# Kernel tuning notes

Hardware: AMD Instinct MI355X
Metric: run time of the kernel (lower is better)

Reference implementation:

```python
import jax, jax.numpy as jnp
import numpy as np

N_NODES = 20000
N_EDGES = 640000
IN_DIM = 128
HEADS = 4
C1 = 64      # hidden_dim1
C2 = 128     # hidden_dim2 (gat2, 1 head)
GRU = 128
PW = 15      # pred_window


def gat_layer(x, src, dst, W, a_src, a_dst, bias):
    # PyG GATConv (eval mode, self-loops already appended): linear -> per-edge
    # LeakyReLU(0.2) attention -> segment softmax over dst -> scatter-sum.
    n = x.shape[0]
    heads, ch = a_src.shape
    xl = (x @ W).reshape(n, heads, ch)                      # [N,H,C]
    al = jnp.sum(xl * a_src, axis=-1)                       # [N,H]
    ar = jnp.sum(xl * a_dst, axis=-1)                       # [N,H]
    e = jax.nn.leaky_relu(al[src] + ar[dst], 0.2)           # [E,H]
    m = jax.ops.segment_max(e, dst, num_segments=n)
    ee = jnp.exp(e - m[dst])
    s = jax.ops.segment_sum(ee, dst, num_segments=n)
    alpha = ee / s[dst]                                     # [E,H]
    msg = xl[src] * alpha[:, :, None]                       # [E,H,C]
    out = jax.ops.segment_sum(msg, dst, num_segments=n)
    return out.reshape(n, heads * ch) + bias


def gru_cell(x, h, W_ih, W_hh, b_ih, b_hh):
    gi = x @ W_ih.T + b_ih
    gh = h @ W_hh.T + b_hh
    ir, iz, ih = jnp.split(gi, 3, axis=1)
    hr, hz, hn = jnp.split(gh, 3, axis=1)
    r = jax.nn.sigmoid(ir + hr)
    z = jax.nn.sigmoid(iz + hz)
    n = jnp.tanh(ih + r * hn)
    return (1.0 - z) * n + z * h


def setup_inputs() -> dict:
    key = jax.random.key(0)
    ks = jax.random.split(key, 24)
    f = jnp.float32
    sc = 0.05
    inp = {
        'dynamic': jax.random.normal(ks[0], (N_NODES, IN_DIM), dtype=f),
        'edge_index': jax.random.randint(ks[1], (2, N_EDGES), 0, N_NODES, dtype=jnp.int32),
        'cI': jax.random.uniform(ks[2], (N_NODES,), dtype=f),
        'cR': jax.random.uniform(ks[3], (N_NODES,), dtype=f),
        'Npop': jnp.ones((N_NODES, 1), dtype=f) * 1e6,
        'I': jax.random.uniform(ks[4], (N_NODES,), dtype=f) * 100.0,
        'R': jax.random.uniform(ks[5], (N_NODES,), dtype=f) * 100.0,
        'dI': jax.random.normal(ks[6], (N_NODES,), dtype=f),
        'dR': jax.random.normal(ks[7], (N_NODES,), dtype=f),
        # gat1
        'W1': jax.random.normal(ks[8], (IN_DIM, HEADS * C1), dtype=f) * sc,
        'a_src1': jax.random.normal(ks[9], (HEADS, C1), dtype=f) * sc,
        'a_dst1': jax.random.normal(ks[10], (HEADS, C1), dtype=f) * sc,
        'b1': jnp.zeros((HEADS * C1,), dtype=f),
        # gat2 (1 head)
        'W2': jax.random.normal(ks[11], (HEADS * C1, C2), dtype=f) * sc,
        'a_src2': jax.random.normal(ks[12], (1, C2), dtype=f) * sc,
        'a_dst2': jax.random.normal(ks[13], (1, C2), dtype=f) * sc,
        'b2': jnp.zeros((C2,), dtype=f),
        # GRUCell
        'W_ih': jax.random.normal(ks[14], (3 * GRU, C2), dtype=f) * sc,
        'W_hh': jax.random.normal(ks[15], (3 * GRU, GRU), dtype=f) * sc,
        'b_ih': jnp.zeros((3 * GRU,), dtype=f),
        'b_hh': jnp.zeros((3 * GRU,), dtype=f),
        # output heads
        'W_I': jax.random.normal(ks[16], (PW, GRU + 2), dtype=f) * sc,
        'b_I': jnp.zeros((PW,), dtype=f),
        'W_R': jax.random.normal(ks[17], (PW, GRU + 2), dtype=f) * sc,
        'b_R': jnp.zeros((PW,), dtype=f),
        'W_sir': jax.random.normal(ks[18], (2, GRU + 2), dtype=f) * sc,
        'b_sir': jnp.zeros((2,), dtype=f),
    }
    return inp


def reference(dynamic, edge_index, cI, cR, Npop, I, R, dI, dR,
              W1, a_src1, a_dst1, b1, W2, a_src2, a_dst2, b2,
              W_ih, W_hh, b_ih, b_hh, W_I, b_I, W_R, b_R, W_sir, b_sir):
    n = dynamic.shape[0]
    loops = jnp.arange(n, dtype=edge_index.dtype)
    src = jnp.concatenate([edge_index[0], loops])   # PyG add_self_loops=True
    dst = jnp.concatenate([edge_index[1], loops])

    x = jax.nn.elu(gat_layer(dynamic, src, dst, W1, a_src1, a_dst1, b1))
    x = jax.nn.elu(gat_layer(x, src, dst, W2, a_src2, a_dst2, b2))

    h = gru_cell(x, jnp.zeros((n, GRU), dtype=x.dtype), W_ih, W_hh, b_ih, b_hh)
    hc = jnp.concatenate([h, cI[:, None], cR[:, None]], axis=1)
    pred_I = hc @ W_I.T + b_I
    pred_R = hc @ W_R.T + b_R
    pred_res = hc @ W_sir.T + b_sir
    alpha = jax.nn.sigmoid(pred_res[:, 0])
    beta = jax.nn.sigmoid(pred_res[:, 1])

    Nv = Npop[:, 0]
    S = Nv - I - R
    phy_I, phy_R = [], []
    for _ in range(PW):
        dI_val = alpha * I * (S / Nv) - beta * I
        dR_val = beta * I
        phy_I.append(dI_val)
        phy_R.append(dR_val)
        I = I + jax.lax.stop_gradient(dI_val)
        R = R + jax.lax.stop_gradient(dR_val)
    phy_I = jnp.stack(phy_I, axis=1)
    phy_R = jnp.stack(phy_R, axis=1)
    return pred_I, pred_R, phy_I, phy_R, h
```

## Files before the change

kernel.cpp:

```cpp
#include <hip/hip_runtime.h>

#define NN 20000
#define NE 640000
#define NET (NE + NN)
#define NB 128
#define RR 157
#define NSL 256
#define ESL4 625

typedef __attribute__((ext_vector_type(8))) short bf16x8;
typedef __attribute__((ext_vector_type(4))) float f32x4;
typedef __attribute__((ext_vector_type(2))) float f32x2;

__device__ inline ushort f2bf_rne(float x) {
    unsigned u = __float_as_uint(x);
    return (ushort)((u + 0x7FFFu + ((u >> 16) & 1u)) >> 16);
}
__device__ inline float bf2f(ushort u) {
    return __uint_as_float(((unsigned)u) << 16);
}
__device__ inline void split2(float x, ushort& hi, ushort& lo) {
    unsigned u = __float_as_uint(x);
    unsigned r = (u + 0x7FFFu + ((u >> 16) & 1u)) & 0xFFFF0000u;
    hi = (ushort)(r >> 16);
    lo = f2bf_rne(x - __uint_as_float(r));
}
__device__ inline float rlane(float x, int k) {
    return __int_as_float(__builtin_amdgcn_readlane(__float_as_int(x), k));
}


__global__ void csrA_kernel(const int* __restrict__ ei, int* __restrict__ cnt,
                            const float* __restrict__ W1, const float* __restrict__ as1,
                            const float* __restrict__ ad1, float* __restrict__ w1f,
                            const float* __restrict__ W2, const float* __restrict__ as2,
                            const float* __restrict__ ad2, float* __restrict__ w2f,
                            const float* __restrict__ W_ih,
                            const float* __restrict__ W_I, const float* __restrict__ b_I,
                            const float* __restrict__ W_R, const float* __restrict__ b_R,
                            const float* __restrict__ W_sir, const float* __restrict__ b_sir,
                            ushort* __restrict__ w1fh, ushort* __restrict__ w1fl,
                            ushort* __restrict__ w2fh, ushort* __restrict__ w2fl,
                            ushort* __restrict__ w3fh, ushort* __restrict__ w3fl,
                            ushort* __restrict__ wtfh, ushort* __restrict__ wtfl,
                            float* __restrict__ wc, float* __restrict__ wb) {
    int b = blockIdx.x, t = threadIdx.x;
    if (b < NSL) {
        __shared__ int h[NB];
        if (t < NB) h[t] = 0;
        __syncthreads();
        const int4* d4 = (const int4*)(ei + NE);
        for (int i = t; i < ESL4; i += 256) {
            int4 d = d4[b * ESL4 + i];
            atomicAdd(&h[(unsigned)d.x / RR], 1);
            atomicAdd(&h[(unsigned)d.y / RR], 1);
            atomicAdd(&h[(unsigned)d.z / RR], 1);
            atomicAdd(&h[(unsigned)d.w / RR], 1);
        }
        __syncthreads();
        if (t < NB) cnt[t * NSL + b] = h[t];
    } else if (b == NSL) {
        if (t < 128) {
            int k = t;
#pragma unroll
            for (int hh = 0; hh < 4; hh++) {
                float s1 = 0.f, s2 = 0.f;
                for (int c = 0; c < 64; c++) {
                    float w = W1[k * 256 + hh * 64 + c];
                    s1 += w * as1[hh * 64 + c];
                    s2 += w * ad1[hh * 64 + c];
                }
                w1f[k * 8 + hh] = s1;
                w1f[k * 8 + 4 + hh] = s2;
            }
        }
    } else if (b == NSL + 1) {
        int k = t;
        float s1 = 0.f, s2 = 0.f;
        for (int c = 0; c < 128; c++) {
            float w = W2[k * 128 + c];
            s1 += w * as2[c];
            s2 += w * ad2[c];
        }
        w2f[k * 2] = s1;
        w2f[k * 2 + 1] = s2;
    } else if (b == NSL + 2) {
        if (t < 32) {
            int p = t;
            const float* Wr = (p < 15) ? W_I + p * 130
                            : (p < 30) ? W_R + (p - 15) * 130
                                       : W_sir + (p - 30) * 130;
            wc[p * 2] = Wr[128];
            wc[p * 2 + 1] = Wr[129];
            wb[p] = (p < 15) ? b_I[p] : (p < 30) ? b_R[p - 15] : b_sir[p - 30];
        }
    } else {
        int pb = b - (NSL + 3);
        if (pb < 16) {
            int base = pb * 2048;
#pragma unroll
            for (int q = 0; q < 8; q++) {
                int i = base + t + q * 256;
                int j = i & 7, ln = (i >> 3) & 63, rem = i >> 9;
                int k32 = rem & 3, n16 = rem >> 2;
                int k = k32 * 32 + ((ln >> 4) << 3) + j;
                int n = n16 * 16 + (ln & 15);
                ushort h, l; split2(W1[k * 256 + n], h, l);
                w1fh[i] = h; w1fl[i] = l;
            }
        } else if (pb < 32) {
            int base = (pb - 16) * 2048;
#pragma unroll
            for (int q = 0; q < 8; q++) {
                int i = base + t + q * 256;
                int j = i & 7, ln = (i >> 3) & 63, rem = i >> 9;
                int k32 = rem & 7, n16 = rem >> 3;
                int k = k32 * 32 + ((ln >> 4) << 3) + j;
                int n = n16 * 16 + (ln & 15);
                ushort h, l; split2(W2[k * 128 + n], h, l);
                w2fh[i] = h; w2fl[i] = l;
            }
        } else if (pb < 56) {
            int base = (pb - 32) * 2048;
#pragma unroll
            for (int q = 0; q < 8; q++) {
                int i = base + t + q * 256;
                int j = i & 7, ln = (i >> 3) & 63, rem = i >> 9;
                int k32 = rem & 3, n16 = rem >> 2;
                int k = k32 * 32 + ((ln >> 4) << 3) + j;
                int n = n16 * 16 + (ln & 15);
                ushort h, l; split2(W_ih[n * 128 + k], h, l);
                w3fh[i] = h; w3fl[i] = l;
            }
        } else {
            int base = (pb - 56) * 2048;
#pragma unroll
            for (int q = 0; q < 8; q++) {
                int i = base + t + q * 256;
                int j = i & 7, ln = (i >> 3) & 63, rem = i >> 9;
                int k32 = rem & 3, n16 = rem >> 2;
                int k = k32 * 32 + ((ln >> 4) << 3) + j;
                int n = n16 * 16 + (ln & 15);
                const float* Wr = (n < 15) ? W_I + n * 130
                                : (n < 30) ? W_R + (n - 15) * 130
                                           : W_sir + (n - 30) * 130;
                ushort h, l; split2(Wr[k], h, l);
                wtfh[i] = h; wtfl[i] = l;
            }
        }
    }
}

__global__ void csrB_kernel(const int* __restrict__ cnt, int* __restrict__ sbase) {
    __shared__ int ws1[16], ws2[16];
    int t = threadIdx.x, wv = t >> 6, ln = t & 63;
    int base = t * 32;
    int loc[32];
    int run = 0;
#pragma unroll
    for (int q = 0; q < 32; q++) { loc[q] = run; run += cnt[base + q]; }
    int s = run;
#pragma unroll
    for (int o = 1; o < 64; o <<= 1) { int u = __shfl_up(s, o, 64); if (ln >= o) s += u; }
    if (ln == 63) ws1[wv] = s;
    __syncthreads();
    if (t < 16) {
        int sv = ws1[t];
#pragma unroll
        for (int o = 1; o < 16; o <<= 1) { int u = __shfl_up(sv, o, 16); if (t >= o) sv += u; }
        ws2[t] = sv;
    }
    __syncthreads();
    int excl = (wv ? ws2[wv - 1] : 0) + s - run;
#pragma unroll
    for (int q = 0; q < 32; q++) sbase[base + q] = excl + loc[q];
}

__global__ void csrC_kernel(const int* __restrict__ ei, const int* __restrict__ sbase,
                            int* __restrict__ ebuf, const float* __restrict__ X,
                            const float* __restrict__ wf, ushort* __restrict__ Xbf,
                            float* __restrict__ al, float* __restrict__ ar) {
    int b = blockIdx.x, t = threadIdx.x;
    if (b < NSL) {
        __shared__ int cur[NB];
        if (t < NB) cur[t] = sbase[t * NSL + b];
        __syncthreads();
        const int4* s4 = (const int4*)ei;
        const int4* d4 = (const int4*)(ei + NE);
        for (int i = t; i < ESL4; i += 256) {
            int4 sv = s4[b * ESL4 + i];
            int4 dv = d4[b * ESL4 + i];
            int p;
            p = atomicAdd(&cur[(unsigned)dv.x / RR], 1); ebuf[p] = sv.x | (dv.x << 15);
            p = atomicAdd(&cur[(unsigned)dv.y / RR], 1); ebuf[p] = sv.y | (dv.y << 15);
            p = atomicAdd(&cur[(unsigned)dv.z / RR], 1); ebuf[p] = sv.z | (dv.z << 15);
            p = atomicAdd(&cur[(unsigned)dv.w / RR], 1); ebuf[p] = sv.w | (dv.w << 15);
        }
    } else {
        __shared__ float ws[8][128];
        for (int i = t; i < 1024; i += 256) ws[i & 7][i >> 3] = wf[i];
        __syncthreads();
        int wv = t >> 6, ln = t & 63;
        int n = (b - NSL) * 4 + wv;
        float2 xv = *(const float2*)(X + (size_t)n * 128 + ln * 2);
        ushort2 ub;
        ub.x = f2bf_rne(xv.x);
        ub.y = f2bf_rne(xv.y);
        *(ushort2*)(Xbf + (size_t)n * 128 + ln * 2) = ub;
        float p[8];
#pragma unroll
        for (int o = 0; o < 8; o++) p[o] = xv.x * ws[o][ln * 2] + xv.y * ws[o][ln * 2 + 1];
#pragma unroll
        for (int off = 32; off > 0; off >>= 1)
#pragma unroll
            for (int o = 0; o < 8; o++) p[o] += __shfl_xor(p[o], off, 64);
        if (ln == 0) {
#pragma unroll
            for (int h = 0; h < 4; h++) {
                al[n * 4 + h] = p[h];
                ar[n * 4 + h] = p[4 + h];
            }
        }
    }
}

__global__ void csrD_kernel(const int* __restrict__ ebuf, const int* __restrict__ sbase,
                            int* __restrict__ offs, int* __restrict__ csr_src) {
    __shared__ int hist[RR], lcur[RR];
    int b = blockIdx.x, t = threadIdx.x;
    int lo = b * RR;
    int Ra = min(RR, NN - lo);
    int e0 = sbase[b * NSL];
    int e1 = (b < NB - 1) ? sbase[(b + 1) * NSL] : NE;
    int m = e1 - e0;
    for (int i = t; i < Ra; i += 256) hist[i] = 0;
    __syncthreads();
    for (int j = t; j < m; j += 256) atomicAdd(&hist[(ebuf[e0 + j] >> 15) - lo], 1);
    __syncthreads();
    if (t < 64) {
        int cbase = e0 + lo;
        int carry = 0;
#pragma unroll
        for (int c = 0; c < 3; c++) {
            int i = c * 64 + t;
            int v = (i < Ra) ? hist[i] + 1 : 0;
            int s = v;
#pragma unroll
            for (int o = 1; o < 64; o <<= 1) { int u = __shfl_up(s, o, 64); if (t >= o) s += u; }
            if (i < Ra) {
                int off = cbase + carry + s - v;
                offs[lo + i] = off;
                lcur[i] = off;
            }
            carry += __shfl(s, 63, 64);
        }
    }
    if (b == 0 && t == 255) offs[NN] = NET;
    __syncthreads();
    for (int i = t; i < Ra; i += 256) csr_src[lcur[i] + hist[i]] = lo + i;
    __syncthreads();
    for (int j = t; j < m; j += 256) {
        int p = ebuf[e0 + j];
        int pos = atomicAdd(&lcur[(p >> 15) - lo], 1);
        csr_src[pos] = p & 0x7FFF;
    }
}

template <int H, bool FUSE>
__launch_bounds__(256)
__global__ void gat_gather_w(const ushort* __restrict__ X, const float* __restrict__ al,
                             const float* __restrict__ ar, const int* __restrict__ offs,
                             const int* __restrict__ csr, const float* __restrict__ bias,
                             void* __restrict__ outp) {
    int t = threadIdx.x;
    int wv = t >> 6, ln = t & 63;
    int n = blockIdx.x * 4 + wv;
    int e0 = offs[n], e1 = offs[n + 1];

    float arv[H], srun[H];
    f32x2 acc2[H];
#pragma unroll
    for (int h = 0; h < H; h++) {
        arv[h] = ar[n * H + h];
        srun[h] = 0.f;
        acc2[h][0] = 0.f; acc2[h][1] = 0.f;
    }
    const ushort* Xc = X + ln * 2;

    for (int base = e0; base < e1; base += 64) {
        int cnt = e1 - base; if (cnt > 64) cnt = 64;
        bool vld = ln < cnt;
        int src = vld ? csr[base + ln] : 0;
        float wgt[H];
        {
            float av[H];
            if (H == 4) {
                float4 a4 = *(const float4*)(al + (size_t)src * 4);
                av[0] = a4.x; av[H > 1 ? 1 : 0] = a4.y;
                av[H > 2 ? 2 : 0] = a4.z; av[H > 3 ? 3 : 0] = a4.w;
            } else {
                av[0] = al[src];
            }
#pragma unroll
            for (int h = 0; h < H; h++) {
                float lg = av[h] + arv[h];
                lg = lg > 0.f ? lg : 0.2f * lg;
                wgt[h] = vld ? __expf(lg) : 0.f;
            }
        }
        float ls[H];
#pragma unroll
        for (int h = 0; h < H; h++) ls[h] = wgt[h];
#pragma unroll
        for (int off = 32; off > 0; off >>= 1)
#pragma unroll
            for (int h = 0; h < H; h++) ls[h] += __shfl_xor(ls[h], off, 64);
#pragma unroll
        for (int h = 0; h < H; h++) srun[h] += ls[h];

        int k = 0;
        for (; k + 16 <= cnt; k += 16) {
            int s[16];
            unsigned u[16];
#pragma unroll
            for (int q = 0; q < 16; q++) s[q] = __builtin_amdgcn_readlane(src, k + q);
#pragma unroll
            for (int q = 0; q < 16; q++) u[q] = *(const unsigned*)(Xc + (size_t)s[q] * 128);
#pragma unroll
            for (int q = 0; q < 16; q++) {
                f32x2 xv;
                xv[0] = __uint_as_float(u[q] << 16);
                xv[1] = __uint_as_float(u[q] & 0xffff0000u);
#pragma unroll
                for (int h = 0; h < H; h++) {
                    float w = rlane(wgt[h], k + q);
                    f32x2 ww; ww[0] = w; ww[1] = w;
                    acc2[h] = __builtin_elementwise_fma(ww, xv, acc2[h]);
                }
            }
        }
        for (; k + 8 <= cnt; k += 8) {
            int s[8];
            unsigned u[8];
#pragma unroll
            for (int q = 0; q < 8; q++) s[q] = __builtin_amdgcn_readlane(src, k + q);
#pragma unroll
            for (int q = 0; q < 8; q++) u[q] = *(const unsigned*)(Xc + (size_t)s[q] * 128);
#pragma unroll
            for (int q = 0; q < 8; q++) {
                f32x2 xv;
                xv[0] = __uint_as_float(u[q] << 16);
                xv[1] = __uint_as_float(u[q] & 0xffff0000u);
#pragma unroll
                for (int h = 0; h < H; h++) {
                    float w = rlane(wgt[h], k + q);
                    f32x2 ww; ww[0] = w; ww[1] = w;
                    acc2[h] = __builtin_elementwise_fma(ww, xv, acc2[h]);
                }
            }
        }
        for (; k < cnt; k++) {
            int s0 = __builtin_amdgcn_readlane(src, k);
            unsigned u0 = *(const unsigned*)(Xc + (size_t)s0 * 128);
            f32x2 xv;
            xv[0] = __uint_as_float(u0 << 16);
            xv[1] = __uint_as_float(u0 & 0xffff0000u);
#pragma unroll
            for (int h = 0; h < H; h++) {
                float w = rlane(wgt[h], k);
                f32x2 ww; ww[0] = w; ww[1] = w;
                acc2[h] = __builtin_elementwise_fma(ww, xv, acc2[h]);
            }
        }
    }
    if (FUSE) {
        ushort* out = (ushort*)outp;
        float inv = 1.f / srun[0];
        float v0 = acc2[0][0] * inv + bias[ln * 2];
        float v1 = acc2[0][1] * inv + bias[ln * 2 + 1];
        v0 = v0 > 0.f ? v0 : __expf(v0) - 1.f;
        v1 = v1 > 0.f ? v1 : __expf(v1) - 1.f;
        ushort2 o;
        o.x = f2bf_rne(v0);
        o.y = f2bf_rne(v1);
        *(ushort2*)(out + (size_t)n * 128 + ln * 2) = o;
    } else {
        ushort* out = (ushort*)outp;
#pragma unroll
        for (int h = 0; h < H; h++) {
            float inv = 1.f / srun[h];
            ushort2 o;
            o.x = f2bf_rne(acc2[h][0] * inv);
            o.y = f2bf_rne(acc2[h][1] * inv);
            *(ushort2*)(out + (size_t)n * (H * 128) + h * 128 + ln * 2) = o;
        }
    }
}

template <int ACT, bool OUTBF, int BN, bool ALAR>
__launch_bounds__(256)
__global__ void gemm_fr(const ushort* __restrict__ A, const ushort* __restrict__ Bfh,
                        const ushort* __restrict__ Bfl, const float* __restrict__ bias,
                        void* __restrict__ Cptr, int M, int K, int lda, int ldc,
                        int zA, int zB, int zC, const float* __restrict__ w2f,
                        float* __restrict__ al2, float* __restrict__ ar2) {
    constexpr int NF = BN / 32;
    __shared__ ushort Ah[128 * 64];
    __shared__ float s_w2f[ALAR ? 256 : 1][2];
    int tid = threadIdx.x;
    int z = blockIdx.z;
    int bm = blockIdx.x * 128;
    int ny = blockIdx.y * BN;
    int wid = tid >> 6, ln = tid & 63;
    int wm = wid >> 1, wn = wid & 1;
    int K32v = K >> 5;
    const bf16x8* BfhV = (const bf16x8*)Bfh;
    const bf16x8* BflV = (const bf16x8*)Bfl;
    f32x4 acc[4][NF];
#pragma unroll
    for (int a = 0; a < 4; a++)
#pragma unroll
        for (int b = 0; b < NF; b++)
#pragma unroll
            for (int j = 0; j < 4; j++) acc[a][b][j] = 0.f;
    float p0a[8], p1a[8];
    if (ALAR) {
#pragma unroll
        for (int i = 0; i < 8; i++) { p0a[i] = 0.f; p1a[i] = 0.f; }
        s_w2f[tid][0] = w2f[tid * 2];
        s_w2f[tid][1] = w2f[tid * 2 + 1];
        __syncthreads();
    }
    size_t abase = (size_t)z * zA;
    int bcb = z * zB + ny;
    int ct[NF];
#pragma unroll
    for (int nf = 0; nf < NF; nf++) ct[nf] = (bcb + wn * (BN / 2) + nf * 16) >> 4;

    for (int k0 = 0; k0 < K; k0 += 64) {
#pragma unroll
        for (int i = 0; i < 8; i++) {
            int idx = tid + i * 256;
            int r = idx >> 4, c4 = (idx & 15) * 4;
            int gr = bm + r;
            ushort4 v = make_ushort4(0, 0, 0, 0);
            if (gr < M) v = *(const ushort4*)(A + abase + (size_t)gr * lda + k0 + c4);
            int ab = (r * 128 + c4 * 2) ^ ((r & 7) << 4);
            *(ushort4*)((char*)Ah + ab) = v;
            if (ALAR) {
                int kk = k0 + c4;
                float x0 = bf2f(v.x), x1 = bf2f(v.y), x2 = bf2f(v.z), x3 = bf2f(v.w);
                p0a[i] = fmaf(x0, s_w2f[kk][0], p0a[i]);
                p0a[i] = fmaf(x1, s_w2f[kk + 1][0], p0a[i]);
                p0a[i] = fmaf(x2, s_w2f[kk + 2][0], p0a[i]);
                p0a[i] = fmaf(x3, s_w2f[kk + 3][0], p0a[i]);
                p1a[i] = fmaf(x0, s_w2f[kk][1], p1a[i]);
                p1a[i] = fmaf(x1, s_w2f[kk + 1][1], p1a[i]);
                p1a[i] = fmaf(x2, s_w2f[kk + 2][1], p1a[i]);
                p1a[i] = fmaf(x3, s_w2f[kk + 3][1], p1a[i]);
            }
        }
        __syncthreads();
#pragma unroll
        for (int ks = 0; ks < 2; ks++) {
            int k32 = (k0 >> 5) + ks;
            int kb = ks * 64 + (ln >> 4) * 16;
            bf16x8 ah[4];
#pragma unroll
            for (int mf = 0; mf < 4; mf++) {
                int r = wm * 64 + mf * 16 + (ln & 15);
                int ab = (r * 128 + kb) ^ ((r & 7) << 4);
                ah[mf] = *(bf16x8*)((char*)Ah + ab);
            }
#pragma unroll
            for (int nf = 0; nf < NF; nf++) {
                size_t fb = (size_t)(ct[nf] * K32v + k32) * 64 + ln;
                bf16x8 bh = BfhV[fb];
                bf16x8 bl = BflV[fb];
#pragma unroll
                for (int mf = 0; mf < 4; mf++) {
                    acc[mf][nf] = __builtin_amdgcn_mfma_f32_16x16x32_bf16(ah[mf], bh, acc[mf][nf], 0, 0, 0);
                    acc[mf][nf] = __builtin_amdgcn_mfma_f32_16x16x32_bf16(ah[mf], bl, acc[mf][nf], 0, 0, 0);
                }
            }
        }
        __syncthreads();
    }
    if (ALAR) {
#pragma unroll
        for (int i = 0; i < 8; i++) {
            float p0 = p0a[i], p1 = p1a[i];
#pragma unroll
            for (int off = 8; off > 0; off >>= 1) {
                p0 += __shfl_xor(p0, off, 16);
                p1 += __shfl_xor(p1, off, 16);
            }
            if ((tid & 15) == 0) {
                int gr = bm + (tid >> 4) + i * 16;
                if (gr < M) { al2[gr] = p0; ar2[gr] = p1; }
            }
        }
    }
    float* Cf = (float*)Cptr;
    ushort* Cu = (ushort*)Cptr;
#pragma unroll
    for (int mf = 0; mf < 4; mf++)
#pragma unroll
        for (int nf = 0; nf < NF; nf++) {
            int colL = ny + wn * (BN / 2) + nf * 16 + (ln & 15);
#pragma unroll
            for (int j = 0; j < 4; j++) {
                int row = bm + wm * 64 + mf * 16 + (ln >> 4) * 4 + j;
                if (row < M) {
                    float v = acc[mf][nf][j];
                    if (ACT) {
                        v += bias[z * zC + colL];
                        v = v > 0.f ? v : (__expf(v) - 1.f);
                    }
                    size_t ci = (size_t)row * ldc + z * zC + colL;
                    if (OUTBF) Cu[ci] = f2bf_rne(v);
                    else       Cf[ci] = v;
                }
            }
        }
}

__launch_bounds__(256)
__global__ void tail_kernel(const ushort* __restrict__ gi, const float* __restrict__ b_ih,
                            const float* __restrict__ b_hh, const ushort* __restrict__ wtfh,
                            const ushort* __restrict__ wtfl, const float* __restrict__ wc,
                            const float* __restrict__ wb, const float* __restrict__ cI,
                            const float* __restrict__ cR, const float* __restrict__ Npop,
                            const float* __restrict__ I0, const float* __restrict__ R0,
                            float* __restrict__ out_h, float* __restrict__ predI,
                            float* __restrict__ predR, float* __restrict__ phyI,
                            float* __restrict__ phyR) {
    __shared__ ushort As[64 * 128];
    __shared__ float s_ab[2][64];
    __shared__ float s_ci[64], s_cr[64];
    int t = threadIdx.x;
    int bm = blockIdx.x * 64;
    int wid = t >> 6, ln = t & 63;
    const bf16x8* WTh = (const bf16x8*)wtfh;
    const bf16x8* WTl = (const bf16x8*)wtfl;
    if (t < 64) {
        int n = bm + t;
        s_ci[t] = (n < NN) ? cI[n] : 0.f;
        s_cr[t] = (n < NN) ? cR[n] : 0.f;
    }
    for (int i = t; i < 2048; i += 256) {
        int r = i >> 5, c4 = (i & 31) * 4;
        int n = bm + r;
        ushort4 ua = make_ushort4(0, 0, 0, 0), ub = ua, uc = ua;
        if (n < NN) {
            const ushort* g = gi + (size_t)n * 384;
            ua = *(const ushort4*)(g + c4);
            ub = *(const ushort4*)(g + 128 + c4);
            uc = *(const ushort4*)(g + 256 + c4);
        }
        float gaa[4] = {bf2f(ua.x), bf2f(ua.y), bf2f(ua.z), bf2f(ua.w)};
        float gba[4] = {bf2f(ub.x), bf2f(ub.y), bf2f(ub.z), bf2f(ub.w)};
        float gca[4] = {bf2f(uc.x), bf2f(uc.y), bf2f(uc.z), bf2f(uc.w)};
        float hv[4];
#pragma unroll
        for (int q = 0; q < 4; q++) {
            int c = c4 + q;
            float rr = 1.f / (1.f + __expf(-(gaa[q] + b_ih[c] + b_hh[c])));
            float zz = 1.f / (1.f + __expf(-(gba[q] + b_ih[128 + c] + b_hh[128 + c])));
            float xx = gca[q] + b_ih[256 + c] + rr * b_hh[256 + c];
            xx = fminf(fmaxf(xx, -15.f), 15.f);
            float e2 = __expf(2.f * xx);
            hv[q] = (1.f - zz) * (e2 - 1.f) / (e2 + 1.f);
        }
        if (n < NN)
            *(float4*)(out_h + (size_t)n * 128 + c4) = make_float4(hv[0], hv[1], hv[2], hv[3]);
        ushort4 hb = make_ushort4(f2bf_rne(hv[0]), f2bf_rne(hv[1]), f2bf_rne(hv[2]), f2bf_rne(hv[3]));
        int ab = (r * 256 + c4 * 2) ^ ((r & 7) << 4);
        *(ushort4*)((char*)As + ab) = hb;
    }
    __syncthreads();
    f32x4 acc2[2];
#pragma unroll
    for (int nf = 0; nf < 2; nf++)
#pragma unroll
        for (int j = 0; j < 4; j++) acc2[nf][j] = 0.f;
#pragma unroll
    for (int ks = 0; ks < 4; ks++) {
        int r = wid * 16 + (ln & 15);
        int abyte = (r * 256 + ks * 64 + (ln >> 4) * 16) ^ ((r & 7) << 4);
        bf16x8 ah = *(bf16x8*)((char*)As + abyte);
#pragma unroll
        for (int nf = 0; nf < 2; nf++) {
            size_t fb = (size_t)(nf * 4 + ks) * 64 + ln;
            bf16x8 bh = WTh[fb];
            bf16x8 bl = WTl[fb];
            acc2[nf] = __builtin_amdgcn_mfma_f32_16x16x32_bf16(ah, bh, acc2[nf], 0, 0, 0);
            acc2[nf] = __builtin_amdgcn_mfma_f32_16x16x32_bf16(ah, bl, acc2[nf], 0, 0, 0);
        }
    }
#pragma unroll
    for (int nf = 0; nf < 2; nf++) {
        int col = nf * 16 + (ln & 15);
#pragma unroll
        for (int j = 0; j < 4; j++) {
            int rl = wid * 16 + (ln >> 4) * 4 + j;
            int n = bm + rl;
            float v = acc2[nf][j] + s_ci[rl] * wc[col * 2] + s_cr[rl] * wc[col * 2 + 1] + wb[col];
            if (n < NN) {
                if (col < 15)      predI[(size_t)n * 15 + col] = v;
                else if (col < 30) predR[(size_t)n * 15 + col - 15] = v;
            }
            if (col == 30) s_ab[0][rl] = v;
            if (col == 31) s_ab[1][rl] = v;
        }
    }
    __syncthreads();
    if (t < 64) {
        int n = bm + t;
        if (n < NN) {
            float alpha = 1.f / (1.f + __expf(-s_ab[0][t]));
            float beta  = 1.f / (1.f + __expf(-s_ab[1][t]));
            float Nv = Npop[n];
            float Iv = I0[n], Rv = R0[n];
            float SoN = (Nv - Iv - Rv) / Nv;
            for (int st = 0; st < 15; st++) {
                float dI = alpha * Iv * SoN - beta * Iv;
                float dR = beta * Iv;
                phyI[(size_t)n * 15 + st] = dI;
                phyR[(size_t)n * 15 + st] = dR;
                Iv += dI; Rv += dR;
            }
        }
    }
}

extern "C" void kernel_launch(void* const* d_in, const int* in_sizes, int n_in,
                              void* d_out, int out_size, void* d_ws, size_t ws_size,
                              hipStream_t stream) {
    const float* dynamic = (const float*)d_in[0];
    const int*   ei      = (const int*)d_in[1];
    const float* cI      = (const float*)d_in[2];
    const float* cR      = (const float*)d_in[3];
    const float* Npop    = (const float*)d_in[4];
    const float* I0      = (const float*)d_in[5];
    const float* R0      = (const float*)d_in[6];
    const float* W1      = (const float*)d_in[9];
    const float* a_src1  = (const float*)d_in[10];
    const float* a_dst1  = (const float*)d_in[11];
    const float* b1      = (const float*)d_in[12];
    const float* W2      = (const float*)d_in[13];
    const float* a_src2  = (const float*)d_in[14];
    const float* a_dst2  = (const float*)d_in[15];
    const float* b2      = (const float*)d_in[16];
    const float* W_ih    = (const float*)d_in[17];
    const float* b_ih    = (const float*)d_in[19];
    const float* b_hh    = (const float*)d_in[20];
    const float* W_I     = (const float*)d_in[21];
    const float* b_I     = (const float*)d_in[22];
    const float* W_R     = (const float*)d_in[23];
    const float* b_R     = (const float*)d_in[24];
    const float* W_sir   = (const float*)d_in[25];
    const float* b_sir   = (const float*)d_in[26];
    float* out = (float*)d_out;
    float* out_predI = out;
    float* out_predR = out + 300000;
    float* out_phyI  = out + 600000;
    float* out_phyR  = out + 900000;
    float* out_h     = out + 1200000;

    int* wsi = (int*)d_ws;
    int* offs    = wsi;
    int* csr_src = wsi + 20096;
    int* cnt     = wsi + 680192;
    int* sbase   = wsi + 712960;
    float* fp = (float*)(wsi + 745728);
    float* w1f = fp; fp += 1152;
    float* w2f = fp; fp += 512;
    float* wc  = fp; fp += 64;
    float* wb  = fp; fp += 64;
    float* al1 = fp; fp += 80128;
    float* ar1 = fp; fp += 80128;
    float* al2 = fp; fp += 20096;
    float* ar2 = fp; fp += 20096;
    ushort* wub  = (ushort*)fp; fp += 118784;
    ushort* w1fh = wub;
    ushort* w1fl = wub + 32768;
    ushort* w2fh = wub + 65536;
    ushort* w2fl = wub + 98304;
    ushort* w3fh = wub + 131072;
    ushort* w3fl = wub + 180224;
    ushort* wtfh = wub + 229376;
    ushort* wtfl = wub + 233472;
    ushort* dyn_bf = (ushort*)fp; fp += 1280000;
    ushort* x1u = (ushort*)fp; fp += 2560000;
    ushort* x2u = x1u;
    float* R  = fp; fp += 7680000;
    int* ebuf = (int*)R;
    ushort* agg_bf = (ushort*)R;
    ushort* xl2_bf = (ushort*)R;
    ushort* gi_bf  = (ushort*)R;

    csrA_kernel<<<NSL + 3 + 58, 256, 0, stream>>>(ei, cnt, W1, a_src1, a_dst1, w1f,
                                                  W2, a_src2, a_dst2, w2f, W_ih,
                                                  W_I, b_I, W_R, b_R, W_sir, b_sir,
                                                  w1fh, w1fl, w2fh, w2fl, w3fh, w3fl,
                                                  wtfh, wtfl, wc, wb);
    csrB_kernel<<<1, 1024, 0, stream>>>(cnt, sbase);
    csrC_kernel<<<NSL + 5000, 256, 0, stream>>>(ei, sbase, ebuf, dynamic, w1f,
                                                dyn_bf, al1, ar1);
    csrD_kernel<<<NB, 256, 0, stream>>>(ebuf, sbase, offs, csr_src);

    gat_gather_w<4, false><<<5000, 256, 0, stream>>>(dyn_bf, al1, ar1, offs, csr_src, nullptr, agg_bf);
    gemm_fr<1, true, 64, false><<<dim3(157, 1, 4), 256, 0, stream>>>(
        agg_bf, w1fh, w1fl, b1, x1u, NN, 128, 512, 256, 128, 64, 64,
        nullptr, nullptr, nullptr);

    gemm_fr<0, true, 128, true><<<dim3(157, 1, 1), 256, 0, stream>>>(
        x1u, w2fh, w2fl, nullptr, xl2_bf, NN, 256, 256, 128, 0, 0, 0,
        w2f, al2, ar2);
    gat_gather_w<1, true><<<5000, 256, 0, stream>>>(xl2_bf, al2, ar2, offs, csr_src, b2, x2u);

    gemm_fr<0, true, 128, false><<<dim3(157, 3, 1), 256, 0, stream>>>(
        x2u, w3fh, w3fl, nullptr, gi_bf, NN, 128, 128, 384, 0, 0, 0,
        nullptr, nullptr, nullptr);

    tail_kernel<<<313, 256, 0, stream>>>(gi_bf, b_ih, b_hh, wtfh, wtfl, wc, wb,
                                         cI, cR, Npop, I0, R0, out_h,
                                         out_predI, out_predR, out_phyI, out_phyR);
}
```

Before: 192.1 us.

## Shrink GEMM tiles to 64x64 and double CSR destination bucket count

The split-bf16 MFMA GEMM moves from 128xBN tiles, where each wave holds a 64xBN/2 sub-tile, to 64x64 tiles where each wave owns one 16-column strip. The grid grows along M and N, which launches more blocks and lowers register and LDS use per block so more blocks fit on each CU. In exchange, each A tile is loaded more times across N blocks, and the al/ar projection is done only by blocks with y==0. Separately, the CSR bucketing goes from 128 buckets of 157 nodes to 256 buckets of 79, so each csrD block handles less work and there is more parallelism, while the prefix scan in csrB handles twice as many counters.

```diff
diff --git a/kernel.cpp b/kernel.cpp
--- a/kernel.cpp
+++ b/kernel.cpp
@@ -3,8 +3,8 @@
 #define NN 20000
 #define NE 640000
 #define NET (NE + NN)
-#define NB 128
-#define RR 157
+#define NB 256
+#define RR 79
 #define NSL 256
 #define ESL4 625
 
@@ -47,7 +47,7 @@
     int b = blockIdx.x, t = threadIdx.x;
     if (b < NSL) {
         __shared__ int h[NB];
-        if (t < NB) h[t] = 0;
+        h[t] = 0;
         __syncthreads();
         const int4* d4 = (const int4*)(ei + NE);
         for (int i = t; i < ESL4; i += 256) {
@@ -58,7 +58,7 @@
             atomicAdd(&h[(unsigned)d.w / RR], 1);
         }
         __syncthreads();
-        if (t < NB) cnt[t * NSL + b] = h[t];
+        cnt[t * NSL + b] = h[t];
     } else if (b == NSL) {
         if (t < 128) {
             int k = t;
@@ -154,11 +154,11 @@
 __global__ void csrB_kernel(const int* __restrict__ cnt, int* __restrict__ sbase) {
     __shared__ int ws1[16], ws2[16];
     int t = threadIdx.x, wv = t >> 6, ln = t & 63;
-    int base = t * 32;
-    int loc[32];
+    int base = t * 64;
+    int loc[64];
     int run = 0;
 #pragma unroll
-    for (int q = 0; q < 32; q++) { loc[q] = run; run += cnt[base + q]; }
+    for (int q = 0; q < 64; q++) { loc[q] = run; run += cnt[base + q]; }
     int s = run;
 #pragma unroll
     for (int o = 1; o < 64; o <<= 1) { int u = __shfl_up(s, o, 64); if (ln >= o) s += u; }
@@ -173,7 +173,7 @@
     __syncthreads();
     int excl = (wv ? ws2[wv - 1] : 0) + s - run;
 #pragma unroll
-    for (int q = 0; q < 32; q++) sbase[base + q] = excl + loc[q];
+    for (int q = 0; q < 64; q++) sbase[base + q] = excl + loc[q];
 }
 
 __global__ void csrC_kernel(const int* __restrict__ ei, const int* __restrict__ sbase,
@@ -183,7 +183,7 @@
     int b = blockIdx.x, t = threadIdx.x;
     if (b < NSL) {
         __shared__ int cur[NB];
-        if (t < NB) cur[t] = sbase[t * NSL + b];
+        cur[t] = sbase[t * NSL + b];
         __syncthreads();
         const int4* s4 = (const int4*)ei;
         const int4* d4 = (const int4*)(ei + NE);
@@ -230,6 +230,7 @@
     int b = blockIdx.x, t = threadIdx.x;
     int lo = b * RR;
     int Ra = min(RR, NN - lo);
+    if (Ra <= 0) { if (b == 0 && t == 255) offs[NN] = NET; return; }
     int e0 = sbase[b * NSL];
     int e1 = (b < NB - 1) ? sbase[(b + 1) * NSL] : NE;
     int m = e1 - e0;
@@ -241,7 +242,7 @@
         int cbase = e0 + lo;
         int carry = 0;
 #pragma unroll
-        for (int c = 0; c < 3; c++) {
+        for (int c = 0; c < 2; c++) {
             int i = c * 64 + t;
             int v = (i < Ra) ? hist[i] + 1 : 0;
             int s = v;
@@ -397,49 +398,43 @@
     }
 }
 
-template <int ACT, bool OUTBF, int BN, bool ALAR>
+template <int ACT, bool OUTBF, bool ALAR>
 __launch_bounds__(256)
 __global__ void gemm_fr(const ushort* __restrict__ A, const ushort* __restrict__ Bfh,
                         const ushort* __restrict__ Bfl, const float* __restrict__ bias,
                         void* __restrict__ Cptr, int M, int K, int lda, int ldc,
                         int zA, int zB, int zC, const float* __restrict__ w2f,
                         float* __restrict__ al2, float* __restrict__ ar2) {
-    constexpr int NF = BN / 32;
-    __shared__ ushort Ah[128 * 64];
+    __shared__ ushort Ah[64 * 64];
     __shared__ float s_w2f[ALAR ? 256 : 1][2];
     int tid = threadIdx.x;
     int z = blockIdx.z;
-    int bm = blockIdx.x * 128;
-    int ny = blockIdx.y * BN;
+    int bm = blockIdx.x * 64;
+    int ny = blockIdx.y * 64;
     int wid = tid >> 6, ln = tid & 63;
-    int wm = wid >> 1, wn = wid & 1;
     int K32v = K >> 5;
     const bf16x8* BfhV = (const bf16x8*)Bfh;
     const bf16x8* BflV = (const bf16x8*)Bfl;
-    f32x4 acc[4][NF];
+    f32x4 acc[4];
 #pragma unroll
     for (int a = 0; a < 4; a++)
 #pragma unroll
-        for (int b = 0; b < NF; b++)
-#pragma unroll
-            for (int j = 0; j < 4; j++) acc[a][b][j] = 0.f;
-    float p0a[8], p1a[8];
+        for (int j = 0; j < 4; j++) acc[a][j] = 0.f;
+    float p0a[4], p1a[4];
+    bool do_alar = ALAR && blockIdx.y == 0;
     if (ALAR) {
 #pragma unroll
-        for (int i = 0; i < 8; i++) { p0a[i] = 0.f; p1a[i] = 0.f; }
+        for (int i = 0; i < 4; i++) { p0a[i] = 0.f; p1a[i] = 0.f; }
         s_w2f[tid][0] = w2f[tid * 2];
         s_w2f[tid][1] = w2f[tid * 2 + 1];
         __syncthreads();
     }
     size_t abase = (size_t)z * zA;
-    int bcb = z * zB + ny;
-    int ct[NF];
-#pragma unroll
-    for (int nf = 0; nf < NF; nf++) ct[nf] = (bcb + wn * (BN / 2) + nf * 16) >> 4;
+    int ct = (z * zB + ny + wid * 16) >> 4;
 
     for (int k0 = 0; k0 < K; k0 += 64) {
 #pragma unroll
-        for (int i = 0; i < 8; i++) {
+        for (int i = 0; i < 4; i++) {
             int idx = tid + i * 256;
             int r = idx >> 4, c4 = (idx & 15) * 4;
             int gr = bm + r;
@@ -447,7 +442,7 @@
             if (gr < M) v = *(const ushort4*)(A + abase + (size_t)gr * lda + k0 + c4);
             int ab = (r * 128 + c4 * 2) ^ ((r & 7) << 4);
             *(ushort4*)((char*)Ah + ab) = v;
-            if (ALAR) {
+            if (ALAR && do_alar) {
                 int kk = k0 + c4;
                 float x0 = bf2f(v.x), x1 = bf2f(v.y), x2 = bf2f(v.z), x3 = bf2f(v.w);
                 p0a[i] = fmaf(x0, s_w2f[kk][0], p0a[i]);
@@ -465,30 +460,23 @@
         for (int ks = 0; ks < 2; ks++) {
             int k32 = (k0 >> 5) + ks;
             int kb = ks * 64 + (ln >> 4) * 16;
-            bf16x8 ah[4];
+            size_t fb = (size_t)(ct * K32v + k32) * 64 + ln;
+            bf16x8 bh = BfhV[fb];
+            bf16x8 bl = BflV[fb];
 #pragma unroll
             for (int mf = 0; mf < 4; mf++) {
-                int r = wm * 64 + mf * 16 + (ln & 15);
+                int r = mf * 16 + (ln & 15);
                 int ab = (r * 128 + kb) ^ ((r & 7) << 4);
-                ah[mf] = *(bf16x8*)((char*)Ah + ab);
-            }
-#pragma unroll
-            for (int nf = 0; nf < NF; nf++) {
-                size_t fb = (size_t)(ct[nf] * K32v + k32) * 64 + ln;
-                bf16x8 bh = BfhV[fb];
-                bf16x8 bl = BflV[fb];
-#pragma unroll
-                for (int mf = 0; mf < 4; mf++) {
-                    acc[mf][nf] = __builtin_amdgcn_mfma_f32_16x16x32_bf16(ah[mf], bh, acc[mf][nf], 0, 0, 0);
-                    acc[mf][nf] = __builtin_amdgcn_mfma_f32_16x16x32_bf16(ah[mf], bl, acc[mf][nf], 0, 0, 0);
-                }
+                bf16x8 ah = *(bf16x8*)((char*)Ah + ab);
+                acc[mf] = __builtin_amdgcn_mfma_f32_16x16x32_bf16(ah, bh, acc[mf], 0, 0, 0);
+                acc[mf] = __builtin_amdgcn_mfma_f32_16x16x32_bf16(ah, bl, acc[mf], 0, 0, 0);
             }
         }
         __syncthreads();
     }
-    if (ALAR) {
-#pragma unroll
-        for (int i = 0; i < 8; i++) {
+    if (ALAR && do_alar) {
+#pragma unroll
+        for (int i = 0; i < 4; i++) {
             float p0 = p0a[i], p1 = p1a[i];
 #pragma unroll
             for (int off = 8; off > 0; off >>= 1) {
@@ -503,26 +491,24 @@
     }
     float* Cf = (float*)Cptr;
     ushort* Cu = (ushort*)Cptr;
-#pragma unroll
-    for (int mf = 0; mf < 4; mf++)
-#pragma unroll
-        for (int nf = 0; nf < NF; nf++) {
-            int colL = ny + wn * (BN / 2) + nf * 16 + (ln & 15);
-#pragma unroll
-            for (int j = 0; j < 4; j++) {
-                int row = bm + wm * 64 + mf * 16 + (ln >> 4) * 4 + j;
-                if (row < M) {
-                    float v = acc[mf][nf][j];
-                    if (ACT) {
-                        v += bias[z * zC + colL];
-                        v = v > 0.f ? v : (__expf(v) - 1.f);
-                    }
-                    size_t ci = (size_t)row * ldc + z * zC + colL;
-                    if (OUTBF) Cu[ci] = f2bf_rne(v);
-                    else       Cf[ci] = v;
+    int colL = ny + wid * 16 + (ln & 15);
+#pragma unroll
+    for (int mf = 0; mf < 4; mf++) {
+#pragma unroll
+        for (int j = 0; j < 4; j++) {
+            int row = bm + mf * 16 + (ln >> 4) * 4 + j;
+            if (row < M) {
+                float v = acc[mf][j];
+                if (ACT) {
+                    v += bias[z * zC + colL];
+                    v = v > 0.f ? v : (__expf(v) - 1.f);
                 }
-            }
-        }
+                size_t ci = (size_t)row * ldc + z * zC + colL;
+                if (OUTBF) Cu[ci] = f2bf_rne(v);
+                else       Cf[ci] = v;
+            }
+        }
+    }
 }
 
 __launch_bounds__(256)
@@ -672,8 +658,8 @@
     int* offs    = wsi;
     int* csr_src = wsi + 20096;
     int* cnt     = wsi + 680192;
-    int* sbase   = wsi + 712960;
-    float* fp = (float*)(wsi + 745728);
+    int* sbase   = wsi + 745728;
+    float* fp = (float*)(wsi + 811264);
     float* w1f = fp; fp += 1152;
     float* w2f = fp; fp += 512;
     float* wc  = fp; fp += 64;
@@ -711,17 +697,17 @@
     csrD_kernel<<<NB, 256, 0, stream>>>(ebuf, sbase, offs, csr_src);
 
     gat_gather_w<4, false><<<5000, 256, 0, stream>>>(dyn_bf, al1, ar1, offs, csr_src, nullptr, agg_bf);
-    gemm_fr<1, true, 64, false><<<dim3(157, 1, 4), 256, 0, stream>>>(
+    gemm_fr<1, true, false><<<dim3(313, 1, 4), 256, 0, stream>>>(
         agg_bf, w1fh, w1fl, b1, x1u, NN, 128, 512, 256, 128, 64, 64,
         nullptr, nullptr, nullptr);
 
-    gemm_fr<0, true, 128, true><<<dim3(157, 1, 1), 256, 0, stream>>>(
+    gemm_fr<0, true, true><<<dim3(313, 2, 1), 256, 0, stream>>>(
         x1u, w2fh, w2fl, nullptr, xl2_bf, NN, 256, 256, 128, 0, 0, 0,
         w2f, al2, ar2);
     gat_gather_w<1, true><<<5000, 256, 0, stream>>>(xl2_bf, al2, ar2, offs, csr_src, b2, x2u);
 
-    gemm_fr<0, true, 128, false><<<dim3(157, 3, 1), 256, 0, stream>>>(
-        x2u, w3fh, w3fl, nullptr, gi_bf, NN, 128, 128, 384, 0, 0, 0,
+    gemm_fr<0, true, false><<<dim3(313, 2, 3), 256, 0, stream>>>(
+        x2u, w3fh, w3fl, nullptr, gi_bf, NN, 128, 128, 384, 0, 128, 128,
         nullptr, nullptr, nullptr);
 
     tail_kernel<<<313, 256, 0, stream>>>(gi_bf, b_ih, b_hh, wtfh, wtfl, wc, wb,
```

Measured after the change: 173.6 us. -9.6%, faster.
